# Performance work log

Measured on AMD Instinct MI355X. Metric: run time of the kernel, lower is better.

Reference implementation:

```python
import jax, jax.numpy as jnp
import numpy as np

N_CLASSES = 20
EPS_DEG = 1e-6
EPS_COS = 1e-8


def setup_inputs() -> dict:
    key = jax.random.key(0)
    k1, k2, k3, k4 = jax.random.split(key, 4)
    S, D, Q = 100, 512, 2048
    support_features = jax.random.normal(k1, (S, D), dtype=jnp.float32)
    support_labels = jnp.repeat(jnp.arange(N_CLASSES, dtype=jnp.int64), S // N_CLASSES)
    query_features = jax.random.normal(k2, (Q, D), dtype=jnp.float32)
    W1 = jax.random.normal(k3, (D, 256), dtype=jnp.float32) * 0.02
    b1 = jnp.zeros((256,), dtype=jnp.float32)
    W2 = jax.random.normal(k4, (256, 128), dtype=jnp.float32) * 0.02
    b2 = jnp.zeros((128,), dtype=jnp.float32)
    return {
        "support_features": support_features,
        "support_labels": support_labels,
        "query_features": query_features,
        "W1": W1, "b1": b1, "W2": W2, "b2": b2,
        "batch_size": 256,
    }


def _build_adj_norm(support_labels, n_support):
    """Symmetrically-normalized adjacency shared by all queries.

    Node 0 = query, nodes 1..S = support. Query <-> every support node;
    support i <-> support j iff same class (includes self-loops on support).
    """
    same = (support_labels[:, None] == support_labels[None, :]).astype(jnp.float32)  # [S,S]
    N = n_support + 1
    adj = jnp.zeros((N, N), dtype=jnp.float32)
    adj = adj.at[0, 1:].set(1.0).at[1:, 0].set(1.0).at[1:, 1:].set(same)
    deg = adj.sum(axis=1)
    dis = (deg + EPS_DEG) ** -0.5
    return dis[:, None] * adj * dis[None, :]


def reference(support_features, support_labels, query_features, W1, b1, W2, b2, batch_size):
    S, D = support_features.shape
    Q = query_features.shape[0]
    C = N_CLASSES

    adj_n = _build_adj_norm(support_labels, S)  # [N,N], query-independent

    # Per-query node features: [Q, N, D] with node 0 = query, 1.. = support
    feats = jnp.concatenate(
        [query_features[:, None, :], jnp.broadcast_to(support_features, (Q, S, D))],
        axis=1,
    )

    # Two GCN layers: h = relu(W(adj_n @ x))
    h = jax.nn.relu(jnp.einsum("nm,qmd->qnd", adj_n, feats) @ W1 + b1)  # [Q,N,256]
    h = jax.nn.relu(jnp.einsum("nm,qmd->qnd", adj_n, h) @ W2 + b2)      # [Q,N,128]

    q_emb = h[:, 0, :]   # [Q,128]
    h_sup = h[:, 1:, :]  # [Q,S,128]

    # Class prototypes: mean of support embeddings per class
    onehot = (support_labels[None, :] == jnp.arange(C)[:, None]).astype(jnp.float32)  # [C,S]
    mean_mat = onehot / onehot.sum(axis=1, keepdims=True)
    protos = jnp.einsum("cs,qsd->qcd", mean_mat, h_sup)  # [Q,C,128]

    # Cosine similarity (torch F.cosine_similarity semantics, eps=1e-8)
    num = jnp.einsum("qd,qcd->qc", q_emb, protos)
    denom = jnp.linalg.norm(q_emb, axis=-1)[:, None] * jnp.linalg.norm(protos, axis=-1)
    return num / jnp.maximum(denom, EPS_COS)  # [Q,C]
```

## Files before the change

### kernel.cpp

```cpp
#include <hip/hip_runtime.h>

#define DD 512
#define H1 256
#define H2 128
#define CC 20
#define CP 24
#define QPB 4
#define MROWS (QPB*CP)
#define PSTR 132
#define NDC 4
#define DCH (DD/NDC)
#define CSB 40

typedef short v8s __attribute__((ext_vector_type(8)));
typedef float v4f __attribute__((ext_vector_type(4)));

#define NSTAT    97
#define OFF_ST2  0
#define OFF_QBC  128
#define OFF_W1F  5248
#define OFF_W2F  70784
#define REQ_FAST 87168
#define OFF_SUMF 0
#define OFF_B1C  10240
#define OFF_H10  16384
#define OFF_PRE  16640
#define OFF_ST   19200
#define OFF_U    19328

static __device__ __forceinline__ unsigned short f2b(float f) {
  union { float f; unsigned int u; } v; v.f = f;
  unsigned int r = v.u + 0x7FFFu + ((v.u >> 16) & 1u);
  return (unsigned short)(r >> 16);
}
static __device__ __forceinline__ float b2f(unsigned short s) {
  union { unsigned int u; float f; } v; v.u = ((unsigned int)s) << 16;
  return v.f;
}

static __device__ __forceinline__ void stats_store(
    const int* __restrict__ labels, int S, float* __restrict__ stats, int t) {
  if (t < CP) {
    int cnt = 0;
    for (int j = 0; j < S; ++j) if (labels[j] == t) cnt++;
    float deg  = 1.f + (float)cnt;
    float dis  = rsqrtf(deg + 1e-6f);
    float dis0 = rsqrtf((float)S + 1e-6f);
    stats[1 + t]          = dis;
    stats[1 + CP + t]     = dis0 * dis;
    stats[1 + 2*CP + t]   = dis * dis * (float)cnt;
    stats[1 + 3*CP + t]   = dis * (float)cnt;
    if (t == 0) stats[0] = dis0;
  }
}

static __device__ __forceinline__ void w1frag_store(
    const float* __restrict__ W1, unsigned short* __restrict__ w1f, int frag, int l) {
  int lr = l & 15, lg = l >> 4;
  int nt = frag >> 4, ks = frag & 15;
  __align__(16) unsigned short o[8];
#pragma unroll
  for (int e = 0; e < 8; ++e)
    o[e] = f2b(W1[(ks * 32 + lg * 8 + e) * H1 + nt * 16 + lr]);
  *(v8s*)&w1f[frag * 512 + l * 8] = *(const v8s*)o;
}

static __device__ __forceinline__ void w2frag_store(
    const float* __restrict__ W2, unsigned short* __restrict__ w2f, int frag, int l) {
  int lr = l & 15, lg = l >> 4;
  int nt = frag >> 3, ks = frag & 7;
  __align__(16) unsigned short o[8];
#pragma unroll
  for (int e = 0; e < 8; ++e)
    o[e] = f2b(W2[(ks * 32 + lg * 8 + e) * H2 + nt * 16 + lr]);
  *(v8s*)&w2f[frag * 512 + l * 8] = *(const v8s*)o;
}

__global__ __launch_bounds__(256) void k_conv2(
    const float* __restrict__ Sf, const int* __restrict__ labels, int S,
    const float* __restrict__ W1, const float* __restrict__ W2,
    unsigned short* __restrict__ qbc, unsigned short* __restrict__ w1f,
    unsigned short* __restrict__ w2f, float* __restrict__ stats) {
  int b = blockIdx.x, t = threadIdx.x;
  if (b < CSB) {
    __shared__ int lab[128];
    if (t < S && t < 128) lab[t] = labels[t];
    __syncthreads();
    int c = b >> 1;
    int d = (b & 1) * 256 + t;
    float acc = 0.f;
    for (int j = 0; j < S; ++j)
      if (lab[j] == c) acc += Sf[(size_t)j * DD + d];
    qbc[c * DD + d] = f2b(acc);
  } else if (b == CSB) {
    stats_store(labels, S, stats, t);
  } else if (b < CSB + 1 + 64) {
    w1frag_store(W1, w1f, (b - CSB - 1) * 4 + (t >> 6), t & 63);
  } else {
    w2frag_store(W2, w2f, (b - CSB - 1 - 64) * 4 + (t >> 6), t & 63);
  }
}

__global__ __launch_bounds__(256) void k_main(
    const float* __restrict__ qf,
    const float* __restrict__ b1, const float* __restrict__ b2,
    const unsigned short* __restrict__ qbc, const unsigned short* __restrict__ w1f,
    const unsigned short* __restrict__ w2f, const float* __restrict__ stats,
    float* __restrict__ out, int Q) {
  __shared__ float smem[MROWS * PSTR];
  __shared__ unsigned short u_all[24 * H1];
  __shared__ float stc[NSTAT];
  __shared__ __align__(16) float b1l[H1];
  __shared__ float b2l[H2];
  __shared__ float qe[QPB * H2];
  __shared__ float qn[QPB];
  unsigned short* ab = (unsigned short*)smem;
  unsigned short* hb = (unsigned short*)smem;
  float* Pm = smem;

  int t = threadIdx.x, q0 = blockIdx.x * QPB;
  if (t < NSTAT) stc[t] = stats[t];
  b1l[t] = b1[t];
  if (t < H2) b2l[t] = b2[t];

  {
    int row = t >> 6, jc = t & 63;
    __align__(16) unsigned short o[8];
    if (q0 + row < Q) {
      const float4 a = *(const float4*)&qf[(size_t)(q0 + row) * DD + jc * 8];
      const float4 c = *(const float4*)&qf[(size_t)(q0 + row) * DD + jc * 8 + 4];
      o[0]=f2b(a.x); o[1]=f2b(a.y); o[2]=f2b(a.z); o[3]=f2b(a.w);
      o[4]=f2b(c.x); o[5]=f2b(c.y); o[6]=f2b(c.z); o[7]=f2b(c.w);
    } else {
#pragma unroll
      for (int e = 0; e < 8; ++e) o[e] = 0;
    }
    *(v8s*)&ab[(row * DD + jc * 8) ^ ((row & 7) << 3)] = *(const v8s*)o;
#pragma unroll
    for (int i = 0; i < 5; ++i) {
      int ch = t + 256 * i;
      int r2 = 4 + (ch >> 6), jc2 = ch & 63;
      v8s v = *(const v8s*)&qbc[(ch >> 6) * DD + jc2 * 8];
      *(v8s*)&ab[(r2 * DD + jc2 * 8) ^ ((r2 & 7) << 3)] = v;
    }
    v8s z = (v8s){0,0,0,0,0,0,0,0};
#pragma unroll
    for (int i = 0; i < 2; ++i) {
      int ch = t + 256 * i;
      int r3 = 24 + (ch >> 6), jc3 = ch & 63;
      *(v8s*)&ab[(r3 * DD + jc3 * 8) ^ ((r3 & 7) << 3)] = z;
    }
  }
  __syncthreads();

  int w = t >> 6, l = t & 63, lr = l & 15, lg = l >> 4;
  {
    v4f ua[2][4];
#pragma unroll
    for (int mt = 0; mt < 2; ++mt)
#pragma unroll
      for (int nt = 0; nt < 4; ++nt) ua[mt][nt] = (v4f){0.f, 0.f, 0.f, 0.f};
#pragma unroll 2
    for (int ks = 0; ks < 16; ++ks) {
      const v8s a0 = *(const v8s*)&ab[((0  + lr) * DD + ks * 32 + lg * 8) ^ ((lr & 7) << 3)];
      const v8s a1 = *(const v8s*)&ab[((16 + lr) * DD + ks * 32 + lg * 8) ^ ((lr & 7) << 3)];
#pragma unroll
      for (int nt = 0; nt < 4; ++nt) {
        const v8s bb = *(const v8s*)&w1f[((w * 4 + nt) * 16 + ks) * 512 + l * 8];
        ua[0][nt] = __builtin_amdgcn_mfma_f32_16x16x32_bf16(a0, bb, ua[0][nt], 0, 0, 0);
        ua[1][nt] = __builtin_amdgcn_mfma_f32_16x16x32_bf16(a1, bb, ua[1][nt], 0, 0, 0);
      }
    }
#pragma unroll
    for (int mt = 0; mt < 2; ++mt)
#pragma unroll
      for (int nt = 0; nt < 4; ++nt)
#pragma unroll
        for (int r = 0; r < 4; ++r) {
          int row = mt * 16 + lg * 4 + r;
          if (row < 24)
            u_all[row * H1 + (w * 4 + nt) * 16 + lr] = f2b(ua[mt][nt][r]);
        }
  }
  __syncthreads();

#pragma unroll 4
  for (int i = 0; i < 12; ++i) {
    int ch = t + 256 * i;
    int r = ch >> 5, jc = ch & 31;
    int q = r / 24, c = r - q * 24;
    int j0 = jc * 8;
    __align__(16) unsigned short o[8];
    if (r == 20) {
      float d0 = stc[0];
#pragma unroll
      for (int e = 0; e < 8; ++e) {
        float s = 0.f;
#pragma unroll
        for (int cc2 = 0; cc2 < CC; ++cc2)
          s = fmaf(stc[1 + cc2], b2f(u_all[(4 + cc2) * H1 + j0 + e]), s);
        o[e] = f2b(fmaxf(fmaf(d0, s, b1l[j0 + e]), 0.f));
      }
    } else {
      int cs = (c < CC) ? c : 0;
      float al = stc[1 + CP + c];
      float dc = stc[1 + cs], sc = dc * dc;
      const v8s uv = *(const v8s*)&u_all[q * H1 + j0];
      const v8s ev = *(const v8s*)&u_all[(4 + cs) * H1 + j0];
#pragma unroll
      for (int e = 0; e < 8; ++e) {
        float u = b2f((unsigned short)uv[e]);
        float x = b2f((unsigned short)ev[e]);
        o[e] = f2b(fmaxf(fmaf(al, u, fmaf(sc, x, b1l[j0 + e])), 0.f));
      }
    }
    *(v8s*)&hb[(r * 256 + j0) ^ ((r & 7) << 3)] = *(const v8s*)o;
  }
  __syncthreads();

  v4f acc[6][2];
#pragma unroll
  for (int mt = 0; mt < 6; ++mt) {
    acc[mt][0] = (v4f){0.f, 0.f, 0.f, 0.f};
    acc[mt][1] = (v4f){0.f, 0.f, 0.f, 0.f};
  }
#pragma unroll
  for (int ks = 0; ks < 8; ++ks) {
    const v8s bb0 = *(const v8s*)&w2f[((w * 2 + 0) * 8 + ks) * 512 + l * 8];
    const v8s bb1 = *(const v8s*)&w2f[((w * 2 + 1) * 8 + ks) * 512 + l * 8];
#pragma unroll
    for (int mt = 0; mt < 6; ++mt) {
      int row = mt * 16 + lr;
      const v8s a = *(const v8s*)&hb[(row * 256 + ks * 32 + lg * 8) ^ ((row & 7) << 3)];
      acc[mt][0] = __builtin_amdgcn_mfma_f32_16x16x32_bf16(a, bb0, acc[mt][0], 0, 0, 0);
      acc[mt][1] = __builtin_amdgcn_mfma_f32_16x16x32_bf16(a, bb1, acc[mt][1], 0, 0, 0);
    }
  }
  __syncthreads();

#pragma unroll
  for (int mt = 0; mt < 6; ++mt)
#pragma unroll
    for (int nt = 0; nt < 2; ++nt)
#pragma unroll
      for (int r = 0; r < 4; ++r)
        Pm[(mt * 16 + lg * 4 + r) * PSTR + (w * 2 + nt) * 16 + lr] = acc[mt][nt][r];
  __syncthreads();

#pragma unroll
  for (int rep = 0; rep < 2; ++rep) {
    int q = (t >> 7) + rep * 2, k = t & 127;
    float s = 0.f;
#pragma unroll
    for (int c = 0; c < CC; ++c) s = fmaf(stc[1 + 3 * CP + c], Pm[(q * 24 + c) * PSTR + k], s);
    qe[q * H2 + k] = fmaxf(fmaf(stc[0], s, b2l[k]), 0.f);
  }
  __syncthreads();

  if (t < 128) {
    int q = t >> 5, ln = t & 31;
    float s = 0.f;
#pragma unroll
    for (int i = 0; i < 4; ++i) { float e = qe[q * H2 + ln + 32 * i]; s = fmaf(e, e, s); }
    s += __shfl_xor(s, 1); s += __shfl_xor(s, 2); s += __shfl_xor(s, 4);
    s += __shfl_xor(s, 8); s += __shfl_xor(s, 16);
    if (ln == 0) qn[q] = s;
  }
  __syncthreads();

#pragma unroll
  for (int rep = 0; rep < 2; ++rep) {
    int q = (t >> 7) + rep * 2;
    int sub = t & 127, c = sub >> 2, lcl = sub & 3;
    if (c < CC && q0 + q < Q) {
      float num = 0.f, pn = 0.f;
      int rowb = (q * 24 + c) * PSTR;
      float bet = stc[1 + 2 * CP + c];
      float d0dc = stc[0] * stc[1 + c];
#pragma unroll
      for (int i = 0; i < 32; ++i) {
        int k = lcl + 4 * i;
        float P = Pm[rowb + k];
        float pr = fmaxf(fmaf(bet, P, fmaf(d0dc, Pm[20 * PSTR + k], b2l[k])), 0.f);
        float e = qe[q * H2 + k];
        num = fmaf(e, pr, num); pn = fmaf(pr, pr, pn);
      }
      num += __shfl_xor(num, 1); pn += __shfl_xor(pn, 1);
      num += __shfl_xor(num, 2); pn += __shfl_xor(pn, 2);
      if (lcl == 0)
        out[(size_t)(q0 + q) * CC + c] = num / fmaxf(sqrtf(qn[q]) * sqrtf(pn), 1e-8f);
    }
  }
}

__global__ __launch_bounds__(256) void k_convfb(
    const float* __restrict__ Sf, const int* __restrict__ labels, int S,
    float* __restrict__ SumF, float* __restrict__ stats) {
  int b = blockIdx.x, t = threadIdx.x;
  if (b < CC) {
    __shared__ int lab[128];
    if (t < S && t < 128) lab[t] = labels[t];
    __syncthreads();
    for (int d = t; d < DD; d += 256) {
      float acc = 0.f;
      for (int j = 0; j < S; ++j)
        if (lab[j] == b) acc += Sf[(size_t)j * DD + d];
      SumF[b * DD + d] = acc;
    }
  } else {
    stats_store(labels, S, stats, t);
  }
}

__global__ __launch_bounds__(256) void k_p2a(
    const float* __restrict__ SumF, const float* __restrict__ W1,
    float* __restrict__ part) {
  int c = blockIdx.x >> 2, dc = blockIdx.x & 3;
  int n = threadIdx.x;
  int d0 = dc * DCH;
  const float* __restrict__ A  = SumF + c * DD + d0;
  const float* __restrict__ Wp = W1 + (size_t)d0 * H1 + n;
  float acc = 0.f;
#pragma unroll 8
  for (int d = 0; d < DCH; ++d)
    acc = fmaf(A[d], Wp[(size_t)d * H1], acc);
  part[(c * NDC + dc) * H1 + n] = acc;
}

__global__ __launch_bounds__(256) void k_p2r(
    const float* __restrict__ part, const float* __restrict__ b1,
    const float* __restrict__ stats, float* __restrict__ B1c,
    float* __restrict__ h10) {
  int b = blockIdx.x, n = threadIdx.x;
  if (b < CC) {
    float dot = part[(b * NDC + 0) * H1 + n] + part[(b * NDC + 1) * H1 + n]
              + part[(b * NDC + 2) * H1 + n] + part[(b * NDC + 3) * H1 + n];
    float dis = stats[1 + b];
    B1c[b * H1 + n] = fmaf(dis * dis, dot, b1[n]);
  } else {
#pragma unroll
    for (int c = CC; c < CP; ++c) B1c[c * H1 + n] = 0.f;
    float s = 0.f;
#pragma unroll 4
    for (int c = 0; c < CC; ++c) {
      float dot = part[(c * NDC + 0) * H1 + n] + part[(c * NDC + 1) * H1 + n]
                + part[(c * NDC + 2) * H1 + n] + part[(c * NDC + 3) * H1 + n];
      s = fmaf(stats[1 + c], dot, s);
    }
    h10[n] = fmaxf(fmaf(stats[0], s, b1[n]), 0.f);
  }
}

__global__ __launch_bounds__(256) void k_pre2(
    const float* __restrict__ h10, const float* __restrict__ W2,
    const float* __restrict__ b2, const float* __restrict__ stats,
    float* __restrict__ pre) {
  __shared__ float red[256];
  int t = threadIdx.x, k = t & 127, jh = t >> 7;
  float g = 0.f;
#pragma unroll 8
  for (int j = jh * 128; j < jh * 128 + 128; ++j)
    g = fmaf(h10[j], W2[j * H2 + k], g);
  red[t] = g;
  __syncthreads();
  if (t < 128) {
    g = red[t] + red[t + 128];
    float d0 = stats[0], bb = b2[k];
#pragma unroll
    for (int c = 0; c < CC; ++c)
      pre[c * H2 + k] = fmaf(d0 * stats[1 + c], g, bb);
  }
}

__global__ __launch_bounds__(256) void k_fb(
    const float* __restrict__ qf, const float* __restrict__ W1,
    const float* __restrict__ W2, const float* __restrict__ b2,
    const float* __restrict__ B1c, const float* __restrict__ pre_ck,
    const float* __restrict__ stats, float* __restrict__ out, int Q) {
  __shared__ __align__(16) float h1[CP][H1];
  __shared__ __align__(16) float proto[CC][H2 + 4];
  __shared__ __align__(16) float psum[8][H2];
  __shared__ float qel[H2];
  __shared__ float stc[NSTAT];
  int tid = threadIdx.x, q = blockIdx.x;
  if (tid < NSTAT) stc[tid] = stats[tid];
  float uvacc = 0.f;
  for (int d = 0; d < DD; ++d) uvacc += qf[(size_t)q * DD + d] * W1[d * H1 + tid];
  __syncthreads();
#pragma unroll
  for (int r = 0; r < CP; ++r)
    h1[r][tid] = fmaxf(stc[1 + CP + r] * uvacc + B1c[r * H1 + tid], 0.f);
  __syncthreads();
  int sg = tid >> 5, kq = tid & 31, k4 = kq * 4, cb = sg * 3;
  float a[3][4];
#pragma unroll
  for (int i = 0; i < 3; ++i)
#pragma unroll
    for (int kk = 0; kk < 4; ++kk) a[i][kk] = 0.f;
  const float4* W2v = (const float4*)W2;
#pragma unroll 2
  for (int j0 = 0; j0 < H1; j0 += 4) {
    float wv[4][4]; float4 hh[3];
#pragma unroll
    for (int jj = 0; jj < 4; ++jj) {
      float4 tv = W2v[(j0 + jj) * 32 + kq];
      wv[jj][0] = tv.x; wv[jj][1] = tv.y; wv[jj][2] = tv.z; wv[jj][3] = tv.w;
    }
#pragma unroll
    for (int i = 0; i < 3; ++i) hh[i] = *(const float4*)&h1[cb + i][j0];
#pragma unroll
    for (int i = 0; i < 3; ++i)
#pragma unroll
      for (int jj = 0; jj < 4; ++jj) {
        float h = ((const float*)&hh[i])[jj];
#pragma unroll
        for (int kk = 0; kk < 4; ++kk) a[i][kk] = fmaf(h, wv[jj][kk], a[i][kk]);
      }
  }
  {
    __align__(16) float part[4] = {0.f, 0.f, 0.f, 0.f};
#pragma unroll
    for (int i = 0; i < 3; ++i) {
      int c = cb + i;
      float gam = stc[1 + 3 * CP + c];
#pragma unroll
      for (int kk = 0; kk < 4; ++kk) part[kk] += gam * a[i][kk];
      if (c < CC) {
        float bet = stc[1 + 2 * CP + c];
        float4 pv = *(const float4*)&pre_ck[c * H2 + k4];
        float4 pr;
        pr.x = fmaxf(pv.x + bet * a[i][0], 0.f);
        pr.y = fmaxf(pv.y + bet * a[i][1], 0.f);
        pr.z = fmaxf(pv.z + bet * a[i][2], 0.f);
        pr.w = fmaxf(pv.w + bet * a[i][3], 0.f);
        *(float4*)&proto[c][k4] = pr;
      }
    }
    *(float4*)&psum[sg][k4] = *(const float4*)part;
  }
  __syncthreads();
  if (tid < H2) {
    float s = 0.f;
#pragma unroll
    for (int g = 0; g < 8; ++g) s += psum[g][tid];
    qel[tid] = fmaxf(stc[0] * s + b2[tid], 0.f);
  }
  __syncthreads();
  if (tid < 160) {
    int c = tid >> 3, ln = tid & 7;
    float num = 0.f, pn = 0.f, qnn = 0.f;
#pragma unroll
    for (int i = 0; i < 16; ++i) {
      int k = ln + 8 * i;
      float e = qel[k], p = proto[c][k];
      num = fmaf(e, p, num); pn = fmaf(p, p, pn); qnn = fmaf(e, e, qnn);
    }
    num += __shfl_xor(num, 1); pn += __shfl_xor(pn, 1); qnn += __shfl_xor(qnn, 1);
    num += __shfl_xor(num, 2); pn += __shfl_xor(pn, 2); qnn += __shfl_xor(qnn, 2);
    num += __shfl_xor(num, 4); pn += __shfl_xor(pn, 4); qnn += __shfl_xor(qnn, 4);
    if (ln == 0)
      out[(size_t)q * CC + c] = num / fmaxf(sqrtf(qnn) * sqrtf(pn), 1e-8f);
  }
}

extern "C" void kernel_launch(void* const* d_in, const int* in_sizes, int n_in,
                              void* d_out, int out_size, void* d_ws, size_t ws_size,
                              hipStream_t stream) {
  const float* Sf     = (const float*)d_in[0];
  const int*   labels = (const int*)d_in[1];
  const float* qf     = (const float*)d_in[2];
  const float* W1     = (const float*)d_in[3];
  const float* b1     = (const float*)d_in[4];
  const float* W2     = (const float*)d_in[5];
  const float* b2     = (const float*)d_in[6];
  int S = in_sizes[1];
  int Q = in_sizes[2] / DD;

  float* ws  = (float*)d_ws;
  float* out = (float*)d_out;

  if (ws_size >= (size_t)REQ_FAST * sizeof(float)) {
    float*          stats = ws + OFF_ST2;
    unsigned short* qbc   = (unsigned short*)(ws + OFF_QBC);
    unsigned short* w1f   = (unsigned short*)(ws + OFF_W1F);
    unsigned short* w2f   = (unsigned short*)(ws + OFF_W2F);
    k_conv2<<<dim3(CSB + 1 + 64 + 16), dim3(256), 0, stream>>>(
        Sf, labels, S, W1, W2, qbc, w1f, w2f, stats);
    k_main<<<dim3((Q + QPB - 1) / QPB), dim3(256), 0, stream>>>(
        qf, b1, b2, qbc, w1f, w2f, stats, out, Q);
  } else {
    float* SumF  = ws + OFF_SUMF;
    float* B1c   = ws + OFF_B1C;
    float* h10   = ws + OFF_H10;
    float* pre   = ws + OFF_PRE;
    float* stats = ws + OFF_ST;
    float* part  = ws + OFF_U;
    k_convfb<<<dim3(CC + 1), dim3(256), 0, stream>>>(Sf, labels, S, SumF, stats);
    k_p2a<<<dim3(CC * NDC), dim3(256), 0, stream>>>(SumF, W1, part);
    k_p2r<<<dim3(CC + 1), dim3(256), 0, stream>>>(part, b1, stats, B1c, h10);
    k_pre2<<<dim3(1), dim3(256), 0, stream>>>(h10, W2, b2, stats, pre);
    k_fb<<<dim3(Q), dim3(256), 0, stream>>>(qf, W1, W2, b2, B1c, pre, stats, out, Q);
  }
}
```

Baseline: 32.02 us.

## Process eight queries per block with 512 threads to amortize shared operand loads

```diff
diff --git a/kernel.cpp b/kernel.cpp
--- a/kernel.cpp
+++ b/kernel.cpp
@@ -5,8 +5,8 @@
 #define H2 128
 #define CC 20
 #define CP 24
-#define QPB 4
-#define MROWS (QPB*CP)
+#define QPB 8
+#define HROWS (QPB*CP)
 #define PSTR 132
 #define NDC 4
 #define DCH (DD/NDC)
@@ -101,14 +101,14 @@
   }
 }
 
-__global__ __launch_bounds__(256) void k_main(
+__global__ __launch_bounds__(512, 1) void k_main(
     const float* __restrict__ qf,
     const float* __restrict__ b1, const float* __restrict__ b2,
     const unsigned short* __restrict__ qbc, const unsigned short* __restrict__ w1f,
     const unsigned short* __restrict__ w2f, const float* __restrict__ stats,
     float* __restrict__ out, int Q) {
-  __shared__ float smem[MROWS * PSTR];
-  __shared__ unsigned short u_all[24 * H1];
+  __shared__ float smem[HROWS * PSTR];
+  __shared__ unsigned short u_all[28 * H1];
   __shared__ float stc[NSTAT];
   __shared__ __align__(16) float b1l[H1];
   __shared__ float b2l[H2];
@@ -120,53 +120,49 @@
 
   int t = threadIdx.x, q0 = blockIdx.x * QPB;
   if (t < NSTAT) stc[t] = stats[t];
-  b1l[t] = b1[t];
-  if (t < H2) b2l[t] = b2[t];
-
-  {
-    int row = t >> 6, jc = t & 63;
+  if (t < H1) b1l[t] = b1[t];
+  if (t >= 128 && t < 256) b2l[t - 128] = b2[t - 128];
+
+#pragma unroll
+  for (int i = 0; i < 4; ++i) {
+    int ch = t + 512 * i;
+    int row = ch >> 6, jc = ch & 63;
     __align__(16) unsigned short o[8];
-    if (q0 + row < Q) {
-      const float4 a = *(const float4*)&qf[(size_t)(q0 + row) * DD + jc * 8];
-      const float4 c = *(const float4*)&qf[(size_t)(q0 + row) * DD + jc * 8 + 4];
-      o[0]=f2b(a.x); o[1]=f2b(a.y); o[2]=f2b(a.z); o[3]=f2b(a.w);
-      o[4]=f2b(c.x); o[5]=f2b(c.y); o[6]=f2b(c.z); o[7]=f2b(c.w);
+    if (row < QPB) {
+      if (q0 + row < Q) {
+        const float4 a = *(const float4*)&qf[(size_t)(q0 + row) * DD + jc * 8];
+        const float4 c = *(const float4*)&qf[(size_t)(q0 + row) * DD + jc * 8 + 4];
+        o[0]=f2b(a.x); o[1]=f2b(a.y); o[2]=f2b(a.z); o[3]=f2b(a.w);
+        o[4]=f2b(c.x); o[5]=f2b(c.y); o[6]=f2b(c.z); o[7]=f2b(c.w);
+      } else {
+#pragma unroll
+        for (int e = 0; e < 8; ++e) o[e] = 0;
+      }
+      *(v8s*)&ab[(row * DD + jc * 8) ^ ((row & 7) << 3)] = *(const v8s*)o;
+    } else if (row < QPB + CC) {
+      v8s v = *(const v8s*)&qbc[(row - QPB) * DD + jc * 8];
+      *(v8s*)&ab[(row * DD + jc * 8) ^ ((row & 7) << 3)] = v;
     } else {
-#pragma unroll
-      for (int e = 0; e < 8; ++e) o[e] = 0;
-    }
-    *(v8s*)&ab[(row * DD + jc * 8) ^ ((row & 7) << 3)] = *(const v8s*)o;
-#pragma unroll
-    for (int i = 0; i < 5; ++i) {
-      int ch = t + 256 * i;
-      int r2 = 4 + (ch >> 6), jc2 = ch & 63;
-      v8s v = *(const v8s*)&qbc[(ch >> 6) * DD + jc2 * 8];
-      *(v8s*)&ab[(r2 * DD + jc2 * 8) ^ ((r2 & 7) << 3)] = v;
-    }
-    v8s z = (v8s){0,0,0,0,0,0,0,0};
-#pragma unroll
-    for (int i = 0; i < 2; ++i) {
-      int ch = t + 256 * i;
-      int r3 = 24 + (ch >> 6), jc3 = ch & 63;
-      *(v8s*)&ab[(r3 * DD + jc3 * 8) ^ ((r3 & 7) << 3)] = z;
+      v8s z = (v8s){0,0,0,0,0,0,0,0};
+      *(v8s*)&ab[(row * DD + jc * 8) ^ ((row & 7) << 3)] = z;
     }
   }
   __syncthreads();
 
   int w = t >> 6, l = t & 63, lr = l & 15, lg = l >> 4;
   {
-    v4f ua[2][4];
+    v4f ua[2][2];
 #pragma unroll
     for (int mt = 0; mt < 2; ++mt)
 #pragma unroll
-      for (int nt = 0; nt < 4; ++nt) ua[mt][nt] = (v4f){0.f, 0.f, 0.f, 0.f};
+      for (int nt = 0; nt < 2; ++nt) ua[mt][nt] = (v4f){0.f, 0.f, 0.f, 0.f};
 #pragma unroll 2
     for (int ks = 0; ks < 16; ++ks) {
       const v8s a0 = *(const v8s*)&ab[((0  + lr) * DD + ks * 32 + lg * 8) ^ ((lr & 7) << 3)];
       const v8s a1 = *(const v8s*)&ab[((16 + lr) * DD + ks * 32 + lg * 8) ^ ((lr & 7) << 3)];
 #pragma unroll
-      for (int nt = 0; nt < 4; ++nt) {
-        const v8s bb = *(const v8s*)&w1f[((w * 4 + nt) * 16 + ks) * 512 + l * 8];
+      for (int nt = 0; nt < 2; ++nt) {
+        const v8s bb = *(const v8s*)&w1f[((w * 2 + nt) * 16 + ks) * 512 + l * 8];
         ua[0][nt] = __builtin_amdgcn_mfma_f32_16x16x32_bf16(a0, bb, ua[0][nt], 0, 0, 0);
         ua[1][nt] = __builtin_amdgcn_mfma_f32_16x16x32_bf16(a1, bb, ua[1][nt], 0, 0, 0);
       }
@@ -174,19 +170,19 @@
 #pragma unroll
     for (int mt = 0; mt < 2; ++mt)
 #pragma unroll
-      for (int nt = 0; nt < 4; ++nt)
+      for (int nt = 0; nt < 2; ++nt)
 #pragma unroll
         for (int r = 0; r < 4; ++r) {
           int row = mt * 16 + lg * 4 + r;
-          if (row < 24)
-            u_all[row * H1 + (w * 4 + nt) * 16 + lr] = f2b(ua[mt][nt][r]);
+          if (row < QPB + CC)
+            u_all[row * H1 + (w * 2 + nt) * 16 + lr] = f2b(ua[mt][nt][r]);
         }
   }
   __syncthreads();
 
 #pragma unroll 4
   for (int i = 0; i < 12; ++i) {
-    int ch = t + 256 * i;
+    int ch = t + 512 * i;
     int r = ch >> 5, jc = ch & 31;
     int q = r / 24, c = r - q * 24;
     int j0 = jc * 8;
@@ -198,7 +194,7 @@
         float s = 0.f;
 #pragma unroll
         for (int cc2 = 0; cc2 < CC; ++cc2)
-          s = fmaf(stc[1 + cc2], b2f(u_all[(4 + cc2) * H1 + j0 + e]), s);
+          s = fmaf(stc[1 + cc2], b2f(u_all[(QPB + cc2) * H1 + j0 + e]), s);
         o[e] = f2b(fmaxf(fmaf(d0, s, b1l[j0 + e]), 0.f));
       }
     } else {
@@ -206,7 +202,7 @@
       float al = stc[1 + CP + c];
       float dc = stc[1 + cs], sc = dc * dc;
       const v8s uv = *(const v8s*)&u_all[q * H1 + j0];
-      const v8s ev = *(const v8s*)&u_all[(4 + cs) * H1 + j0];
+      const v8s ev = *(const v8s*)&u_all[(QPB + cs) * H1 + j0];
 #pragma unroll
       for (int e = 0; e < 8; ++e) {
         float u = b2f((unsigned short)uv[e]);
@@ -218,38 +214,32 @@
   }
   __syncthreads();
 
-  v4f acc[6][2];
-#pragma unroll
-  for (int mt = 0; mt < 6; ++mt) {
-    acc[mt][0] = (v4f){0.f, 0.f, 0.f, 0.f};
-    acc[mt][1] = (v4f){0.f, 0.f, 0.f, 0.f};
-  }
+  v4f acc[12];
+#pragma unroll
+  for (int mt = 0; mt < 12; ++mt) acc[mt] = (v4f){0.f, 0.f, 0.f, 0.f};
 #pragma unroll
   for (int ks = 0; ks < 8; ++ks) {
-    const v8s bb0 = *(const v8s*)&w2f[((w * 2 + 0) * 8 + ks) * 512 + l * 8];
-    const v8s bb1 = *(const v8s*)&w2f[((w * 2 + 1) * 8 + ks) * 512 + l * 8];
-#pragma unroll
-    for (int mt = 0; mt < 6; ++mt) {
+    const v8s bb = *(const v8s*)&w2f[(w * 8 + ks) * 512 + l * 8];
+#pragma unroll
+    for (int mt = 0; mt < 12; ++mt) {
       int row = mt * 16 + lr;
       const v8s a = *(const v8s*)&hb[(row * 256 + ks * 32 + lg * 8) ^ ((row & 7) << 3)];
-      acc[mt][0] = __builtin_amdgcn_mfma_f32_16x16x32_bf16(a, bb0, acc[mt][0], 0, 0, 0);
-      acc[mt][1] = __builtin_amdgcn_mfma_f32_16x16x32_bf16(a, bb1, acc[mt][1], 0, 0, 0);
-    }
-  }
-  __syncthreads();
-
-#pragma unroll
-  for (int mt = 0; mt < 6; ++mt)
-#pragma unroll
-    for (int nt = 0; nt < 2; ++nt)
-#pragma unroll
-      for (int r = 0; r < 4; ++r)
-        Pm[(mt * 16 + lg * 4 + r) * PSTR + (w * 2 + nt) * 16 + lr] = acc[mt][nt][r];
+      acc[mt] = __builtin_amdgcn_mfma_f32_16x16x32_bf16(a, bb, acc[mt], 0, 0, 0);
+    }
+  }
+  __syncthreads();
+
+#pragma unroll
+  for (int mt = 0; mt < 12; ++mt)
+#pragma unroll
+    for (int r = 0; r < 4; ++r)
+      Pm[(mt * 16 + lg * 4 + r) * PSTR + w * 16 + lr] = acc[mt][r];
   __syncthreads();
 
 #pragma unroll
   for (int rep = 0; rep < 2; ++rep) {
-    int q = (t >> 7) + rep * 2, k = t & 127;
+    int idx = t + 512 * rep;
+    int q = idx >> 7, k = idx & 127;
     float s = 0.f;
 #pragma unroll
     for (int c = 0; c < CC; ++c) s = fmaf(stc[1 + 3 * CP + c], Pm[(q * 24 + c) * PSTR + k], s);
@@ -257,7 +247,7 @@
   }
   __syncthreads();
 
-  if (t < 128) {
+  if (t < 256) {
     int q = t >> 5, ln = t & 31;
     float s = 0.f;
 #pragma unroll
@@ -270,8 +260,9 @@
 
 #pragma unroll
   for (int rep = 0; rep < 2; ++rep) {
-    int q = (t >> 7) + rep * 2;
-    int sub = t & 127, c = sub >> 2, lcl = sub & 3;
+    int idx = t + 512 * rep;
+    int q = idx >> 7;
+    int sub = idx & 127, c = sub >> 2, lcl = sub & 3;
     if (c < CC && q0 + q < Q) {
       float num = 0.f, pn = 0.f;
       int rowb = (q * 24 + c) * PSTR;
@@ -486,7 +477,7 @@
     unsigned short* w2f   = (unsigned short*)(ws + OFF_W2F);
     k_conv2<<<dim3(CSB + 1 + 64 + 16), dim3(256), 0, stream>>>(
         Sf, labels, S, W1, W2, qbc, w1f, w2f, stats);
-    k_main<<<dim3((Q + QPB - 1) / QPB), dim3(256), 0, stream>>>(
+    k_main<<<dim3((Q + QPB - 1) / QPB), dim3(512), 0, stream>>>(
         qf, b1, b2, qbc, w1f, w2f, stats, out, Q);
   } else {
     float* SumF  = ws + OFF_SUMF;
```

New measurement: 31.74 us. Within noise of the previous version (-0.9%).
